# Performance work log

Hardware: AMD Instinct MI355X
Metric: run time of the kernel (lower is better)

The kernel has to match this reference:

```python
import jax, jax.numpy as jnp
import numpy as np

N = 8192
E = 131072
NODE_DIM = 128
HIDDEN_DIM = 256


def setup_inputs() -> dict:
    key = jax.random.key(0)
    k1, k2, k3 = jax.random.split(key, 3)
    x = jax.random.normal(k1, (N, NODE_DIM), dtype=jnp.float32)
    edge_index = jax.random.randint(k2, (2, E), 0, N, dtype=jnp.int64)
    # nn.Linear(node_dim, hidden_dim, bias=False): weight [hidden_dim, node_dim]
    W = jax.random.normal(k3, (HIDDEN_DIM, NODE_DIM), dtype=jnp.float32) * (1.0 / np.sqrt(NODE_DIM))
    return {"x": x, "edge_index": edge_index, "W": W}


def reference(x, edge_index, W):
    num_nodes = x.shape[0]
    src, tgt = edge_index[0], edge_index[1]
    # Dense adjacency: A[src, tgt] = 1 (set semantics, duplicates collapse)
    A = jnp.zeros((num_nodes, num_nodes), dtype=x.dtype).at[src, tgt].set(1.0)
    A_tilde = A + jnp.eye(num_nodes, dtype=x.dtype)
    D = A_tilde.sum(axis=1)
    D_inv_sqrt = D ** -0.5
    # D_tilde @ A_tilde @ D_tilde == row/col scaling of A_tilde
    A_hat = D_inv_sqrt[:, None] * A_tilde * D_inv_sqrt[None, :]
    out = A_hat @ x            # [N, node_dim]
    out = out @ W.T            # [N, hidden_dim]
    return out
```

## Files before the change

kernel.cpp:

```cpp
#include <hip/hip_runtime.h>

#define N_NODES 8192
#define NODE_DIM 128
#define HIDDEN_DIM 256
#define WORDS_PER_ROW 256
#define CAP 96

typedef __attribute__((ext_vector_type(8))) short bf16x8;
typedef __attribute__((ext_vector_type(4))) float f32x4;

static __device__ __forceinline__ unsigned short f2bf(float f) {
    unsigned u = __builtin_bit_cast(unsigned, f);
    unsigned r = u + 0x7fffu + ((u >> 16) & 1u);
    return (unsigned short)(r >> 16);
}
static __device__ __forceinline__ float bf2f(unsigned short h) {
    unsigned u = ((unsigned)h) << 16;
    return __builtin_bit_cast(float, u);
}

__global__ void dedupe_kernel(const int* __restrict__ e,
                              unsigned int* __restrict__ bitmask,
                              unsigned int* __restrict__ deg,
                              int* __restrict__ rowlist,
                              const float* __restrict__ W,
                              unsigned short* __restrict__ wh,
                              unsigned short* __restrict__ wl,
                              int E, int nEdgeBlocks) {
    if ((int)blockIdx.x < nEdgeBlocks) {
        int idx = blockIdx.x * 256 + threadIdx.x;
        if (idx >= E) return;
        int s = e[idx];
        int t = e[E + idx];
        unsigned int w = (unsigned int)s * WORDS_PER_ROW + ((unsigned int)t >> 5);
        unsigned int m = 1u << (t & 31);
        unsigned int old = atomicOr(&bitmask[w], m);
        if (!(old & m)) {
            unsigned int p = atomicAdd(&deg[s], 1u);
            if (p < CAP) rowlist[(size_t)s * CAP + p] = t;
        }
    } else {
        int t = (blockIdx.x - nEdgeBlocks) * 256 + threadIdx.x;
        if (t >= HIDDEN_DIM * NODE_DIM / 4) return;
        float4 v = ((const float4*)W)[t];
        ushort4 h, l;
        h.x = f2bf(v.x); l.x = f2bf(v.x - bf2f(h.x));
        h.y = f2bf(v.y); l.y = f2bf(v.y - bf2f(h.y));
        h.z = f2bf(v.z); l.z = f2bf(v.z - bf2f(h.z));
        h.w = f2bf(v.w); l.w = f2bf(v.w - bf2f(h.w));
        ((ushort4*)wh)[t] = h;
        ((ushort4*)wl)[t] = l;
    }
}

__global__ __launch_bounds__(256)
void aggregate_kernel(const int* __restrict__ rowlist,
                      const unsigned int* __restrict__ deg,
                      const float* __restrict__ x,
                      unsigned short* __restrict__ yh,
                      unsigned short* __restrict__ yl) {
    __shared__ int   cols[CAP];
    __shared__ float djs[CAP];
    __shared__ float part[NODE_DIM];
    int i   = blockIdx.x;
    int tid = threadIdx.x;
    int n   = (int)deg[i];
    if (n > CAP) n = CAP;
    if (tid < n) {
        int c = rowlist[(size_t)i * CAP + tid];
        cols[tid] = c;
        djs[tid]  = rsqrtf((float)deg[c] + 1.0f);
    }
    __syncthreads();

    int g = tid >> 7;
    int d = tid & 127;
    float acc = 0.0f;
    for (int k = g; k < n; k += 2) {
        acc += djs[k] * x[(size_t)cols[k] * NODE_DIM + d];
    }
    if (g == 0) part[d] = acc;
    __syncthreads();
    if (g == 1) {
        float di = rsqrtf((float)n + 1.0f);
        float v  = di * (di * x[(size_t)i * NODE_DIM + d] + part[d] + acc);
        unsigned short h = f2bf(v);
        unsigned short l = f2bf(v - bf2f(h));
        yh[(size_t)i * NODE_DIM + d] = h;
        yl[(size_t)i * NODE_DIM + d] = l;
    }
}

__global__ __launch_bounds__(256)
void gemm_kernel(const unsigned short* __restrict__ Yh,
                 const unsigned short* __restrict__ Yl,
                 const unsigned short* __restrict__ Wh,
                 const unsigned short* __restrict__ Wl,
                 float* __restrict__ out) {
    int tid  = threadIdx.x;
    int wave = tid >> 6;
    int lane = tid & 63;
    int quad = lane >> 4;
    int l16  = lane & 15;
    int m0   = blockIdx.y * 64;
    int hcol = blockIdx.x * 64 + wave * 16 + l16;

    const unsigned short* wh_p = Wh + (size_t)hcol * NODE_DIM + quad * 8;
    const unsigned short* wl_p = Wl + (size_t)hcol * NODE_DIM + quad * 8;
    const unsigned short* yh_p = Yh + (size_t)(m0 + l16) * NODE_DIM + quad * 8;
    const unsigned short* yl_p = Yl + (size_t)(m0 + l16) * NODE_DIM + quad * 8;

    f32x4 acc[4] = {{0,0,0,0},{0,0,0,0},{0,0,0,0},{0,0,0,0}};
#pragma unroll
    for (int ks = 0; ks < 4; ++ks) {
        int k = ks * 32;
        bf16x8 bh = *(const bf16x8*)(wh_p + k);
        bf16x8 bl = *(const bf16x8*)(wl_p + k);
#pragma unroll
        for (int mt = 0; mt < 4; ++mt) {
            bf16x8 ah = *(const bf16x8*)(yh_p + k + mt * 16 * NODE_DIM);
            bf16x8 al = *(const bf16x8*)(yl_p + k + mt * 16 * NODE_DIM);
            acc[mt] = __builtin_amdgcn_mfma_f32_16x16x32_bf16(ah, bh, acc[mt], 0, 0, 0);
            acc[mt] = __builtin_amdgcn_mfma_f32_16x16x32_bf16(ah, bl, acc[mt], 0, 0, 0);
            acc[mt] = __builtin_amdgcn_mfma_f32_16x16x32_bf16(al, bh, acc[mt], 0, 0, 0);
        }
    }

#pragma unroll
    for (int mt = 0; mt < 4; ++mt) {
#pragma unroll
        for (int r = 0; r < 4; ++r) {
            out[(size_t)(m0 + mt * 16 + quad * 4 + r) * HIDDEN_DIM + hcol] = acc[mt][r];
        }
    }
}

extern "C" void kernel_launch(void* const* d_in, const int* in_sizes, int n_in,
                              void* d_out, int out_size, void* d_ws, size_t ws_size,
                              hipStream_t stream) {
    const float* x = (const float*)d_in[0];
    const int*   e = (const int*)d_in[1];
    const float* W = (const float*)d_in[2];
    float*       out = (float*)d_out;
    int E = in_sizes[1] / 2;

    unsigned int*   bitmask = (unsigned int*)d_ws;
    unsigned int*   deg     = bitmask + (size_t)N_NODES * WORDS_PER_ROW;
    int*            rowlist = (int*)(deg + N_NODES);
    unsigned short* yh      = (unsigned short*)(rowlist + (size_t)N_NODES * CAP);
    unsigned short* yl      = yh + (size_t)N_NODES * NODE_DIM;
    unsigned short* wh      = yl + (size_t)N_NODES * NODE_DIM;
    unsigned short* wl      = wh + (size_t)HIDDEN_DIM * NODE_DIM;

    size_t clear_bytes = ((size_t)N_NODES * WORDS_PER_ROW + N_NODES) * sizeof(unsigned int);
    hipMemsetAsync(d_ws, 0, clear_bytes, stream);

    int nEdgeBlocks = (E + 255) / 256;
    int nWBlocks    = (HIDDEN_DIM * NODE_DIM / 4 + 255) / 256;
    dedupe_kernel<<<nEdgeBlocks + nWBlocks, 256, 0, stream>>>(e, bitmask, deg, rowlist,
                                                              W, wh, wl, E, nEdgeBlocks);
    aggregate_kernel<<<N_NODES, 256, 0, stream>>>(rowlist, deg, x, yh, yl);
    gemm_kernel<<<dim3(HIDDEN_DIM / 64, N_NODES / 64), 256, 0, stream>>>(yh, yl, wh, wl, out);
}
```

Measured before the change: 104.7 us.

## Fuse aggregation and GEMM into one kernel with LDS-staged rows

Merges the aggregate and GEMM kernels into a single kernel. Each block aggregates 16 rows into shared memory as bf16 hi/lo pairs, then runs MFMA against W for all 256 output columns. This drops the global round trip for the intermediate Y and one kernel launch. In exchange, grid parallelism falls to 512 blocks, each working through 8 serialized aggregation iterations with barriers. W is now reread per block, and the half-block split of each row's neighbor loop is gone.

Result: slower. 107.2 us (+2.4%).

```diff
diff --git a/kernel.cpp b/kernel.cpp
--- a/kernel.cpp
+++ b/kernel.cpp
@@ -5,6 +5,8 @@
 #define HIDDEN_DIM 256
 #define WORDS_PER_ROW 256
 #define CAP 96
+#define MTILE 16
+#define YPAD 136
 
 typedef __attribute__((ext_vector_type(8))) short bf16x8;
 typedef __attribute__((ext_vector_type(4))) float f32x4;
@@ -54,85 +56,73 @@
 }
 
 __global__ __launch_bounds__(256)
-void aggregate_kernel(const int* __restrict__ rowlist,
-                      const unsigned int* __restrict__ deg,
-                      const float* __restrict__ x,
-                      unsigned short* __restrict__ yh,
-                      unsigned short* __restrict__ yl) {
-    __shared__ int   cols[CAP];
-    __shared__ float djs[CAP];
-    __shared__ float part[NODE_DIM];
-    int i   = blockIdx.x;
-    int tid = threadIdx.x;
-    int n   = (int)deg[i];
-    if (n > CAP) n = CAP;
-    if (tid < n) {
-        int c = rowlist[(size_t)i * CAP + tid];
-        cols[tid] = c;
-        djs[tid]  = rsqrtf((float)deg[c] + 1.0f);
+void fused_kernel(const int* __restrict__ rowlist,
+                  const unsigned int* __restrict__ deg,
+                  const float* __restrict__ x,
+                  const unsigned short* __restrict__ wh,
+                  const unsigned short* __restrict__ wl,
+                  float* __restrict__ out) {
+    __shared__ unsigned short yh_lds[MTILE][YPAD];
+    __shared__ unsigned short yl_lds[MTILE][YPAD];
+    __shared__ int   cols[2][CAP];
+    __shared__ float djs[2][CAP];
+
+    int tid  = threadIdx.x;
+    int b    = blockIdx.x;
+    int r0   = b * MTILE;
+    int half = tid >> 7;
+    int t128 = tid & 127;
+
+    for (int iter = 0; iter < MTILE / 2; ++iter) {
+        int s = iter * 2 + half;
+        int i = r0 + s;
+        int n = (int)deg[i];
+        if (n > CAP) n = CAP;
+        if (t128 < n) {
+            int c = rowlist[(size_t)i * CAP + t128];
+            cols[half][t128] = c;
+            djs[half][t128]  = rsqrtf((float)deg[c] + 1.0f);
+        }
+        __syncthreads();
+        float acc = 0.0f;
+        for (int k = 0; k < n; ++k)
+            acc += djs[half][k] * x[(size_t)cols[half][k] * NODE_DIM + t128];
+        float di  = rsqrtf((float)n + 1.0f);
+        float val = di * (di * x[(size_t)i * NODE_DIM + t128] + acc);
+        unsigned short h = f2bf(val);
+        unsigned short l = f2bf(val - bf2f(h));
+        yh_lds[s][t128] = h;
+        yl_lds[s][t128] = l;
+        __syncthreads();
     }
-    __syncthreads();
 
-    int g = tid >> 7;
-    int d = tid & 127;
-    float acc = 0.0f;
-    for (int k = g; k < n; k += 2) {
-        acc += djs[k] * x[(size_t)cols[k] * NODE_DIM + d];
-    }
-    if (g == 0) part[d] = acc;
-    __syncthreads();
-    if (g == 1) {
-        float di = rsqrtf((float)n + 1.0f);
-        float v  = di * (di * x[(size_t)i * NODE_DIM + d] + part[d] + acc);
-        unsigned short h = f2bf(v);
-        unsigned short l = f2bf(v - bf2f(h));
-        yh[(size_t)i * NODE_DIM + d] = h;
-        yl[(size_t)i * NODE_DIM + d] = l;
-    }
-}
-
-__global__ __launch_bounds__(256)
-void gemm_kernel(const unsigned short* __restrict__ Yh,
-                 const unsigned short* __restrict__ Yl,
-                 const unsigned short* __restrict__ Wh,
-                 const unsigned short* __restrict__ Wl,
-                 float* __restrict__ out) {
-    int tid  = threadIdx.x;
     int wave = tid >> 6;
     int lane = tid & 63;
     int quad = lane >> 4;
     int l16  = lane & 15;
-    int m0   = blockIdx.y * 64;
-    int hcol = blockIdx.x * 64 + wave * 16 + l16;
 
-    const unsigned short* wh_p = Wh + (size_t)hcol * NODE_DIM + quad * 8;
-    const unsigned short* wl_p = Wl + (size_t)hcol * NODE_DIM + quad * 8;
-    const unsigned short* yh_p = Yh + (size_t)(m0 + l16) * NODE_DIM + quad * 8;
-    const unsigned short* yl_p = Yl + (size_t)(m0 + l16) * NODE_DIM + quad * 8;
-
-    f32x4 acc[4] = {{0,0,0,0},{0,0,0,0},{0,0,0,0},{0,0,0,0}};
+    f32x4 acc4[4] = {{0,0,0,0},{0,0,0,0},{0,0,0,0},{0,0,0,0}};
 #pragma unroll
     for (int ks = 0; ks < 4; ++ks) {
-        int k = ks * 32;
-        bf16x8 bh = *(const bf16x8*)(wh_p + k);
-        bf16x8 bl = *(const bf16x8*)(wl_p + k);
+        int koff = ks * 32 + quad * 8;
+        bf16x8 ah = *(const bf16x8*)&yh_lds[l16][koff];
+        bf16x8 al = *(const bf16x8*)&yl_lds[l16][koff];
 #pragma unroll
-        for (int mt = 0; mt < 4; ++mt) {
-            bf16x8 ah = *(const bf16x8*)(yh_p + k + mt * 16 * NODE_DIM);
-            bf16x8 al = *(const bf16x8*)(yl_p + k + mt * 16 * NODE_DIM);
-            acc[mt] = __builtin_amdgcn_mfma_f32_16x16x32_bf16(ah, bh, acc[mt], 0, 0, 0);
-            acc[mt] = __builtin_amdgcn_mfma_f32_16x16x32_bf16(ah, bl, acc[mt], 0, 0, 0);
-            acc[mt] = __builtin_amdgcn_mfma_f32_16x16x32_bf16(al, bh, acc[mt], 0, 0, 0);
+        for (int ht = 0; ht < 4; ++ht) {
+            int hcol = wave * 64 + ht * 16 + l16;
+            bf16x8 bh = *(const bf16x8*)(wh + (size_t)hcol * NODE_DIM + koff);
+            bf16x8 bl = *(const bf16x8*)(wl + (size_t)hcol * NODE_DIM + koff);
+            acc4[ht] = __builtin_amdgcn_mfma_f32_16x16x32_bf16(ah, bh, acc4[ht], 0, 0, 0);
+            acc4[ht] = __builtin_amdgcn_mfma_f32_16x16x32_bf16(ah, bl, acc4[ht], 0, 0, 0);
+            acc4[ht] = __builtin_amdgcn_mfma_f32_16x16x32_bf16(al, bh, acc4[ht], 0, 0, 0);
         }
     }
 
 #pragma unroll
-    for (int mt = 0; mt < 4; ++mt) {
+    for (int ht = 0; ht < 4; ++ht)
 #pragma unroll
-        for (int r = 0; r < 4; ++r) {
-            out[(size_t)(m0 + mt * 16 + quad * 4 + r) * HIDDEN_DIM + hcol] = acc[mt][r];
-        }
-    }
+        for (int r = 0; r < 4; ++r)
+            out[(size_t)(r0 + quad * 4 + r) * HIDDEN_DIM + wave * 64 + ht * 16 + l16] = acc4[ht][r];
 }
 
 extern "C" void kernel_launch(void* const* d_in, const int* in_sizes, int n_in,
@@ -147,9 +137,7 @@
     unsigned int*   bitmask = (unsigned int*)d_ws;
     unsigned int*   deg     = bitmask + (size_t)N_NODES * WORDS_PER_ROW;
     int*            rowlist = (int*)(deg + N_NODES);
-    unsigned short* yh      = (unsigned short*)(rowlist + (size_t)N_NODES * CAP);
-    unsigned short* yl      = yh + (size_t)N_NODES * NODE_DIM;
-    unsigned short* wh      = yl + (size_t)N_NODES * NODE_DIM;
+    unsigned short* wh      = (unsigned short*)(rowlist + (size_t)N_NODES * CAP);
     unsigned short* wl      = wh + (size_t)HIDDEN_DIM * NODE_DIM;
 
     size_t clear_bytes = ((size_t)N_NODES * WORDS_PER_ROW + N_NODES) * sizeof(unsigned int);
@@ -159,6 +147,5 @@
     int nWBlocks    = (HIDDEN_DIM * NODE_DIM / 4 + 255) / 256;
     dedupe_kernel<<<nEdgeBlocks + nWBlocks, 256, 0, stream>>>(e, bitmask, deg, rowlist,
                                                               W, wh, wl, E, nEdgeBlocks);
-    aggregate_kernel<<<N_NODES, 256, 0, stream>>>(rowlist, deg, x, yh, yl);
-    gemm_kernel<<<dim3(HIDDEN_DIM / 64, N_NODES / 64), 256, 0, stream>>>(yh, yl, wh, wl, out);
+    fused_kernel<<<N_NODES / MTILE, 256, 0, stream>>>(rowlist, deg, x, wh, wl, out);
 }
```
